# Performance work log

Hardware: AMD Instinct MI355X
Metric: run time of the kernel (lower is better)

The kernel has to match this reference:

```python
import jax, jax.numpy as jnp
import numpy as np

DIM = 2048
N_HEADS = 16
HEAD_DIM = DIM // N_HEADS        # 128
HALF_HD = HEAD_DIM // 2          # 64 (per-context per-head dim)
Q_DIM = DIM // 2                 # 1024
KV_DIM = DIM // 2                # 1024 (n_kv_heads == n_heads)
TOTAL = Q_DIM + 2 * KV_DIM       # 3072
B, S = 2, 2048
EPS = 1e-5


def rmsnorm(x, w, eps=EPS):
    return x * jax.lax.rsqrt(jnp.mean(x * x, axis=-1, keepdims=True) + eps) * w


def rope(x, freqs):
    # x: [B,S,H,D] with D even; freqs: [S, D//2] angles
    xr = x[..., 0::2]
    xi = x[..., 1::2]
    cos = jnp.cos(freqs)[None, :, None, :]
    sin = jnp.sin(freqs)[None, :, None, :]
    out_r = xr * cos - xi * sin
    out_i = xr * sin + xi * cos
    return jnp.stack([out_r, out_i], axis=-1).reshape(x.shape)


def setup_inputs() -> dict:
    key = jax.random.key(0)
    ks = jax.random.split(key, 10)
    inp = {
        "local_c": jax.random.normal(ks[0], (B, S, DIM), jnp.float32),
        "global_c": jax.random.normal(ks[1], (B, S, DIM), jnp.float32),
        "freqs": jax.random.uniform(ks[2], (S, HALF_HD // 2), jnp.float32) * 6.28,
        "W_lc": jax.random.normal(ks[3], (TOTAL, DIM), jnp.float32) * 0.02,
        "W_gc": jax.random.normal(ks[4], (TOTAL, DIM), jnp.float32) * 0.02,
        "q_lc_nw": jnp.ones((Q_DIM,), jnp.float32),
        "k_lc_nw": jnp.ones((KV_DIM,), jnp.float32),
        "q_gc_nw": jnp.ones((Q_DIM,), jnp.float32),
        "k_gc_nw": jnp.ones((KV_DIM,), jnp.float32),
        "q_cat_nw": jnp.ones((HEAD_DIM,), jnp.float32),
        "k_cat_nw": jnp.ones((HEAD_DIM,), jnp.float32),
        "W_lo": jax.random.normal(ks[5], (DIM, 2 * Q_DIM), jnp.float32) * 0.02,
        "b_lo": jnp.zeros((DIM,), jnp.float32),
        "lc_on_w": jnp.ones((DIM,), jnp.float32),
        "W_go": jax.random.normal(ks[6], (DIM, 2 * Q_DIM), jnp.float32) * 0.02,
        "b_go": jnp.zeros((DIM,), jnp.float32),
        "gc_on_w": jnp.ones((DIM,), jnp.float32),
    }
    return inp


def _context_build(x, W, q_nw, k_nw):
    comb = jnp.einsum('bsd,td->bst', x, W)
    q, k, v = jnp.split(comb, [Q_DIM, Q_DIM + KV_DIM], axis=-1)
    q = rmsnorm(q, q_nw).reshape(B, S, N_HEADS, HALF_HD)
    k = rmsnorm(k, k_nw).reshape(B, S, N_HEADS, HALF_HD)
    v = v.reshape(B, S, N_HEADS, HALF_HD)
    return q, k, v


def reference(local_c, global_c, freqs, W_lc, W_gc, q_lc_nw, k_lc_nw, q_gc_nw,
              k_gc_nw, q_cat_nw, k_cat_nw, W_lo, b_lo, lc_on_w, W_go, b_go, gc_on_w):
    q_lc, k_lc, v_lc = _context_build(local_c, W_lc, q_lc_nw, k_lc_nw)
    q_gc, k_gc, v_gc = _context_build(global_c, W_gc, q_gc_nw, k_gc_nw)

    q_lc = rope(q_lc, freqs)
    k_lc = rope(k_lc, freqs)
    q_gc = rope(q_gc, freqs)
    k_gc = rope(k_gc, freqs)

    # concat local+global per head -> [B,S,H,HEAD_DIM], QK-norm over head dim
    xq = rmsnorm(jnp.concatenate([q_lc, q_gc], axis=-1), q_cat_nw)
    xk = rmsnorm(jnp.concatenate([k_lc, k_gc], axis=-1), k_cat_nw)
    xv = jnp.concatenate([v_lc, v_gc], axis=-1)

    scale = 1.0 / np.sqrt(HEAD_DIM)
    scores = jnp.einsum('bqhd,bkhd->bhqk', xq, xk) * scale
    attn = jax.nn.softmax(scores, axis=-1)
    out = jnp.einsum('bhqk,bkhd->bqhd', attn, xv).reshape(B, S, DIM)

    x_lc = rmsnorm(jnp.einsum('bsd,od->bso', out, W_lo) + b_lo, lc_on_w)
    x_gc = rmsnorm(jnp.einsum('bsd,od->bso', out, W_go) + b_go, gc_on_w)
    return (x_lc, x_gc)
```

## Files before the change

### kernel.cpp

```cpp
#include <hip/hip_runtime.h>
#include <hip/hip_bf16.h>

#define DIM 2048
#define NH 16
#define HD 128
#define QD 1024
#define TOT 3072
#define BB 2
#define SS 2048
#define NTOK (BB*SS)
#define EPS 1e-5f

typedef __attribute__((ext_vector_type(4))) float f32x4;
typedef __attribute__((ext_vector_type(8))) short short8;
typedef __attribute__((ext_vector_type(8))) unsigned short u16x8;
typedef __attribute__((ext_vector_type(4))) unsigned short u16x4;

__device__ __forceinline__ float b2f(unsigned short u){
    unsigned int x = ((unsigned int)u) << 16;
    return __builtin_bit_cast(float, x);
}
__device__ __forceinline__ unsigned short f2b(float f){
    unsigned int x = __builtin_bit_cast(unsigned int, f);
    x = (x + 0x7fffu + ((x >> 16) & 1u)) >> 16;
    return (unsigned short)x;
}
__device__ __forceinline__ float exp2_fast(float x){
    float r;
    asm("v_exp_f32 %0, %1" : "=v"(r) : "v"(x));
    return r;
}
__device__ __forceinline__ void store_c(float* p, float v){ *p = v; }
__device__ __forceinline__ void store_c(unsigned short* p, float v){ *p = f2b(v); }

#define MFMA16(a,b,c) __builtin_amdgcn_mfma_f32_16x16x32_bf16((a),(b),(c),0,0,0)

#define GLOAD16(g, l) __builtin_amdgcn_global_load_lds( \
    (const __attribute__((address_space(1))) unsigned int*)(g), \
    (__attribute__((address_space(3))) unsigned int*)(l), 16, 0, 0)

__device__ __forceinline__ void cvt8(const float* __restrict__ s,
                                     unsigned short* __restrict__ d, int i){
    const float4* p = reinterpret_cast<const float4*>(s + (size_t)i * 8);
    float4 a = p[0], b = p[1];
    u16x8 o;
    o[0]=f2b(a.x); o[1]=f2b(a.y); o[2]=f2b(a.z); o[3]=f2b(a.w);
    o[4]=f2b(b.x); o[5]=f2b(b.y); o[6]=f2b(b.z); o[7]=f2b(b.w);
    *reinterpret_cast<u16x8*>(d + (size_t)i * 8) = o;
}

__global__ __launch_bounds__(256) void cvt_multi(
    const float* __restrict__ s0, const float* __restrict__ s1,
    const float* __restrict__ s2, const float* __restrict__ s3,
    const float* __restrict__ s4, const float* __restrict__ s5,
    unsigned short* __restrict__ d0, unsigned short* __restrict__ d1,
    unsigned short* __restrict__ d2, unsigned short* __restrict__ d3,
    unsigned short* __restrict__ d4, unsigned short* __restrict__ d5)
{
    const int N0 = NTOK*DIM/8;
    const int N1 = N0 + NTOK*DIM/8;
    const int N2 = N1 + TOT*DIM/8;
    const int N3 = N2 + TOT*DIM/8;
    const int N4 = N3 + DIM*DIM/8;
    const int N5 = N4 + DIM*DIM/8;
    for (int i = blockIdx.x * blockDim.x + threadIdx.x; i < N5;
         i += gridDim.x * blockDim.x){
        if      (i < N0) cvt8(s0, d0, i);
        else if (i < N1) cvt8(s1, d1, i - N0);
        else if (i < N2) cvt8(s2, d2, i - N1);
        else if (i < N3) cvt8(s3, d3, i - N2);
        else if (i < N4) cvt8(s4, d4, i - N3);
        else             cvt8(s5, d5, i - N4);
    }
}

template<typename OutT>
__global__ __launch_bounds__(256) void gemm_nt(const unsigned short* __restrict__ A0,
                                               const unsigned short* __restrict__ B0,
                                               OutT* __restrict__ C0,
                                               const unsigned short* __restrict__ A1,
                                               const unsigned short* __restrict__ B1,
                                               OutT* __restrict__ C1,
                                               int M, int N, int K){
    __shared__ __attribute__((aligned(16))) unsigned short As[2][128*64];
    __shared__ __attribute__((aligned(16))) unsigned short Bs[2][128*64];
    const int t = threadIdx.x;
    const int lane = t & 63;
    const int w = t >> 6;
    const int wr = w >> 1, wc = w & 1;
    const int gx = gridDim.x;
    const int nwg = gx * gridDim.y;
    int zsel, swz;
    if (gridDim.z == 2){
        const int glin = (int)(blockIdx.z * nwg + blockIdx.y * gx + blockIdx.x);
        const int xcd = glin & 7;
        const int i = glin >> 3;
        zsel = xcd >> 2;
        swz = (xcd & 3) * (nwg >> 2) + i;
    } else {
        const int lin = (int)(blockIdx.y * gx + blockIdx.x);
        const int cpx = nwg >> 3;
        swz = (lin & 7) * cpx + (lin >> 3);
        zsel = 0;
    }
    const unsigned short* A = zsel ? A1 : A0;
    const unsigned short* B = zsel ? B1 : B0;
    OutT* C = zsel ? C1 : C0;
    const int m0 = (swz / gx) * 128, n0 = (swz % gx) * 128;
    const int l16 = lane & 15, lq = lane >> 4;

    f32x4 acc[4][4];
    const f32x4 z = {0.f, 0.f, 0.f, 0.f};
    #pragma unroll
    for (int m = 0; m < 4; ++m)
        #pragma unroll
        for (int n = 0; n < 4; ++n) acc[m][n] = z;

    auto stage = [&](int kt, int bi){
        #pragma unroll
        for (int i = 0; i < 4; ++i){
            int c = t + 256 * i;
            int row = c >> 3, c8 = c & 7;
            int cg = (c8 ^ (row & 7)) * 8;
            GLOAD16(&A[(size_t)(m0 + row) * K + kt + cg],
                    (char*)&As[bi][0] + (size_t)(i * 256 + w * 64) * 16);
            GLOAD16(&B[(size_t)(n0 + row) * K + kt + cg],
                    (char*)&Bs[bi][0] + (size_t)(i * 256 + w * 64) * 16);
        }
    };

    stage(0, 0);
    __syncthreads();
    int cur = 0;

    for (int kt = 0; kt < K; kt += 64){
        if (kt + 64 < K) stage(kt + 64, cur ^ 1);
        #pragma unroll
        for (int kk = 0; kk < 2; ++kk){
            short8 af[4], bf[4];
            #pragma unroll
            for (int m = 0; m < 4; ++m){
                int row = wr*64 + m*16 + l16;
                af[m] = *reinterpret_cast<const short8*>(
                    &As[cur][row*64 + (((kk*4 + lq) ^ (row & 7)) * 8)]);
            }
            #pragma unroll
            for (int n = 0; n < 4; ++n){
                int row = wc*64 + n*16 + l16;
                bf[n] = *reinterpret_cast<const short8*>(
                    &Bs[cur][row*64 + (((kk*4 + lq) ^ (row & 7)) * 8)]);
            }
            #pragma unroll
            for (int m = 0; m < 4; ++m)
                #pragma unroll
                for (int n = 0; n < 4; ++n)
                    acc[m][n] = MFMA16(af[m], bf[n], acc[m][n]);
        }
        __syncthreads();
        cur ^= 1;
    }
    #pragma unroll
    for (int m = 0; m < 4; ++m){
        int grow = m0 + wr*64 + m*16 + lq*4;
        #pragma unroll
        for (int n = 0; n < 4; ++n){
            int gcol = n0 + wc*64 + n*16 + l16;
            #pragma unroll
            for (int r = 0; r < 4; ++r)
                store_c(&C[(size_t)(grow + r) * N + gcol], acc[m][n][r]);
        }
    }
}

__global__ __launch_bounds__(256) void qkv_post(
    const unsigned short* __restrict__ comb_lc, const unsigned short* __restrict__ comb_gc,
    const float* __restrict__ freqs,
    const float* __restrict__ q_lc_nw, const float* __restrict__ k_lc_nw,
    const float* __restrict__ q_gc_nw, const float* __restrict__ k_gc_nw,
    const float* __restrict__ q_cat_nw, const float* __restrict__ k_cat_nw,
    unsigned short* __restrict__ xq, unsigned short* __restrict__ xk,
    unsigned short* __restrict__ xv)
{
    __shared__ float qcat[16][128];
    __shared__ float kcat[16][128];
    __shared__ float rbuf[4][4];
    const int tok = blockIdx.x;
    const int s = tok & (SS - 1);
    const unsigned short* clc = comb_lc + (size_t)tok * TOT;
    const unsigned short* cgc = comb_gc + (size_t)tok * TOT;
    const int t = threadIdx.x;
    const int lane = t & 63, w = t >> 6;

    const unsigned short* segs[4] = { clc, clc + QD, cgc, cgc + QD };
    const float* wts[4] = { q_lc_nw, k_lc_nw, q_gc_nw, k_gc_nw };

    float ss4[4];
    #pragma unroll
    for (int sg = 0; sg < 4; ++sg){
        u16x4 v = *reinterpret_cast<const u16x4*>(segs[sg] + t * 4);
        float acc = 0.f;
        #pragma unroll
        for (int j = 0; j < 4; ++j){ float f = b2f(v[j]); acc += f * f; }
        ss4[sg] = acc;
    }
    #pragma unroll
    for (int sg = 0; sg < 4; ++sg){
        float v = ss4[sg];
        #pragma unroll
        for (int o = 32; o >= 1; o >>= 1) v += __shfl_xor(v, o);
        if (lane == 0) rbuf[sg][w] = v;
    }
    __syncthreads();
    float rms[4];
    #pragma unroll
    for (int sg = 0; sg < 4; ++sg){
        float tot = rbuf[sg][0] + rbuf[sg][1] + rbuf[sg][2] + rbuf[sg][3];
        rms[sg] = rsqrtf(tot * (1.f / QD) + EPS);
    }

    #pragma unroll
    for (int sg = 0; sg < 4; ++sg){
        const unsigned short* seg = segs[sg];
        const float* wt = wts[sg];
        const float rf = rms[sg];
        float (*dst)[128] = (sg == 0 || sg == 2) ? qcat : kcat;
        const int coff = (sg >= 2) ? 64 : 0;
        #pragma unroll
        for (int pi = 0; pi < 2; ++pi){
            int p = t + pi * 256;
            int h = p >> 5, j = p & 31;
            int idx = h * 64 + 2 * j;
            float xr = b2f(seg[idx])     * rf * wt[idx];
            float xi = b2f(seg[idx + 1]) * rf * wt[idx + 1];
            float fr = freqs[(size_t)s * 32 + j];
            float cs = __cosf(fr), sn = __sinf(fr);
            dst[h][coff + 2*j]     = xr * cs - xi * sn;
            dst[h][coff + 2*j + 1] = xr * sn + xi * cs;
        }
    }

    {
        int i0 = t * 4;
        int h = i0 >> 6, d = i0 & 63;
        u16x4 vlc = *reinterpret_cast<const u16x4*>(clc + 2048 + i0);
        u16x4 vgc = *reinterpret_cast<const u16x4*>(cgc + 2048 + i0);
        *reinterpret_cast<u16x4*>(&xv[(size_t)tok * DIM + h * 128 + d])      = vlc;
        *reinterpret_cast<u16x4*>(&xv[(size_t)tok * DIM + h * 128 + 64 + d]) = vgc;
    }
    __syncthreads();

    {
        int h = t >> 4, sub = t & 15;
        float sq = 0.f, sk = 0.f;
        #pragma unroll
        for (int j = 0; j < 8; ++j){
            float a = qcat[h][sub*8 + j]; sq += a * a;
            float b = kcat[h][sub*8 + j]; sk += b * b;
        }
        #pragma unroll
        for (int o = 1; o < 16; o <<= 1){ sq += __shfl_xor(sq, o); sk += __shfl_xor(sk, o); }
        float rq = rsqrtf(sq * (1.f / 128) + EPS);
        float rk = rsqrtf(sk * (1.f / 128) + EPS);
        u16x8 oq, ok;
        #pragma unroll
        for (int j = 0; j < 8; ++j){
            int d = sub*8 + j;
            oq[j] = f2b(qcat[h][d] * rq * q_cat_nw[d]);
            ok[j] = f2b(kcat[h][d] * rk * k_cat_nw[d]);
        }
        *reinterpret_cast<u16x8*>(&xq[(size_t)tok * DIM + h * 128 + sub*8]) = oq;
        *reinterpret_cast<u16x8*>(&xk[(size_t)tok * DIM + h * 128 + sub*8]) = ok;
    }
}

__global__ __launch_bounds__(256) void transpose_v(const unsigned short* __restrict__ xv,
                                                   unsigned short* __restrict__ xvT){
    __shared__ unsigned short tile[128][129];
    const int blk = blockIdx.x;
    const int st = blk & 15;
    const int bh = blk >> 4;
    const int b = bh >> 4, h = bh & 15;
    const int t = threadIdx.x;
    const int s0 = st * 128;
    #pragma unroll
    for (int i = 0; i < 8; ++i){
        int c = t + 256 * i;
        int r = c >> 4, dc = c & 15;
        u16x8 v = *reinterpret_cast<const u16x8*>(&xv[((size_t)(b*SS + s0 + r)) * DIM + h*HD + dc*8]);
        #pragma unroll
        for (int j = 0; j < 8; ++j) tile[r][dc*8 + j] = v[j];
    }
    __syncthreads();
    #pragma unroll
    for (int i = 0; i < 8; ++i){
        int c = t + 256 * i;
        int d = c >> 4, sc = c & 15;
        u16x8 o;
        #pragma unroll
        for (int j = 0; j < 8; ++j) o[j] = tile[sc*8 + j][d];
        *reinterpret_cast<u16x8*>(&xvT[((size_t)bh * HD + d) * SS + s0 + sc*8]) = o;
    }
}

__global__ __launch_bounds__(256) void attn_fwd(const unsigned short* __restrict__ xq,
                                                const unsigned short* __restrict__ xk,
                                                const unsigned short* __restrict__ xvT,
                                                unsigned short* __restrict__ attn_out){
    __shared__ __attribute__((aligned(16))) unsigned short Kl[2][64 * 128];
    __shared__ __attribute__((aligned(16))) unsigned short Vt[2][128 * 64];
    __shared__ __attribute__((aligned(16))) unsigned short Pl[4][16 * 64];
    const int blk = ((int)blockIdx.x & 7) * 128 + ((int)blockIdx.x >> 3);
    const int qt = blk & 31, h = (blk >> 5) & 15, b = blk >> 9;
    const int t = threadIdx.x, lane = t & 63, w = t >> 6;
    const int l16 = lane & 15, lq = lane >> 4;
    const float scale2 = 0.12751744751f;
    const float MBIAS = 16.6f;
    const int qbase = qt * 64 + w * 16;

    short8 qf[4];
    #pragma unroll
    for (int ks = 0; ks < 4; ++ks)
        qf[ks] = *reinterpret_cast<const short8*>(
            &xq[((size_t)(b*SS + qbase + l16)) * DIM + h*HD + ks*32 + lq*8]);

    float psum = 0.f;
    f32x4 O[8];
    const f32x4 z = {0.f, 0.f, 0.f, 0.f};
    #pragma unroll
    for (int dn = 0; dn < 8; ++dn) O[dn] = z;

    const size_t kbase = (size_t)(b*SS) * DIM + h*HD;
    const size_t vbase = ((size_t)(b*NH + h)) * HD * SS;

    auto stage = [&](int kt, int bi){
        #pragma unroll
        for (int i = 0; i < 4; ++i){
            int slot = i*256 + w*64 + lane;
            int r = slot >> 4, dc = slot & 15;
            GLOAD16(&xk[kbase + (size_t)(kt*64 + r) * DIM + ((dc ^ (r & 7)) * 8)],
                    (char*)&Kl[bi][0] + (size_t)(i*256 + w*64) * 16);
            int d = slot >> 3, kc = slot & 7;
            GLOAD16(&xvT[vbase + (size_t)d * SS + kt*64 + ((kc ^ (d & 7)) * 8)],
                    (char*)&Vt[bi][0] + (size_t)(i*256 + w*64) * 16);
        }
    };

    stage(0, 0);
    __syncthreads();

    unsigned short* P = Pl[w];
    int cur = 0;

    for (int kt = 0; kt < SS/64; ++kt){
        if (kt + 1 < SS/64) stage(kt + 1, cur ^ 1);

        const unsigned short* Kc = Kl[cur];
        const unsigned short* Vc = Vt[cur];

        f32x4 St[4];
        #pragma unroll
        for (int kn = 0; kn < 4; ++kn) St[kn] = z;
        __builtin_amdgcn_s_setprio(1);
        #pragma unroll
        for (int kn = 0; kn < 4; ++kn){
            int kr = kn*16 + l16;
            #pragma unroll
            for (int ks = 0; ks < 4; ++ks){
                short8 ak = *reinterpret_cast<const short8*>(
                    &Kc[kr*128 + (((ks*4 + lq) ^ (kr & 7)) * 8)]);
                St[kn] = MFMA16(ak, qf[ks], St[kn]);
            }
        }
        __builtin_amdgcn_s_setprio(0);

        uint2 pk[4];
        #pragma unroll
        for (int kn = 0; kn < 4; ++kn){
            float p0 = exp2_fast(St[kn][0]*scale2 - MBIAS);
            float p1 = exp2_fast(St[kn][1]*scale2 - MBIAS);
            float p2 = exp2_fast(St[kn][2]*scale2 - MBIAS);
            float p3 = exp2_fast(St[kn][3]*scale2 - MBIAS);
            psum += (p0 + p1) + (p2 + p3);
            unsigned lo, hi;
            asm("v_cvt_pk_bf16_f32 %0, %1, %2" : "=v"(lo) : "v"(p0), "v"(p1));
            asm("v_cvt_pk_bf16_f32 %0, %1, %2" : "=v"(hi) : "v"(p2), "v"(p3));
            pk[kn].x = lo; pk[kn].y = hi;
        }

        #pragma unroll
        for (int kn = 0; kn < 4; ++kn){
            int kk = kn >> 1;
            int lqp = (kn & 1)*2 + (lq >> 1);
            *reinterpret_cast<uint2*>(&P[(kk*64 + lqp*16 + l16)*8 + (lq & 1)*4]) = pk[kn];
        }
        asm volatile("s_waitcnt lgkmcnt(0)" ::: "memory");
        __builtin_amdgcn_sched_barrier(0);

        __builtin_amdgcn_s_setprio(1);
        #pragma unroll
        for (int kk = 0; kk < 2; ++kk){
            short8 pb = *reinterpret_cast<const short8*>(&P[(kk*64 + lq*16 + l16)*8]);
            #pragma unroll
            for (int dn = 0; dn < 8; ++dn){
                int dr = dn*16 + l16;
                short8 av = *reinterpret_cast<const short8*>(
                    &Vc[dr*64 + (((kk*4 + lq) ^ (dr & 7)) * 8)]);
                O[dn] = MFMA16(av, pb, O[dn]);
            }
        }
        __builtin_amdgcn_s_setprio(0);

        __syncthreads();
        cur ^= 1;
    }

    psum += __shfl_xor(psum, 16);
    psum += __shfl_xor(psum, 32);
    float inv = 1.f / psum;
    #pragma unroll
    for (int dn = 0; dn < 8; ++dn){
        u16x4 o4;
        #pragma unroll
        for (int r = 0; r < 4; ++r) o4[r] = f2b(O[dn][r] * inv);
        *reinterpret_cast<u16x4*>(
            &attn_out[((size_t)(b*SS + qbase + l16)) * DIM + h*HD + dn*16 + lq*4]) = o4;
    }
}

__global__ __launch_bounds__(256) void proj_norm2(const unsigned short* __restrict__ proj,
                                                  const float* __restrict__ b_lo,
                                                  const float* __restrict__ b_go,
                                                  const float* __restrict__ w_lc,
                                                  const float* __restrict__ w_gc,
                                                  float* __restrict__ out){
    __shared__ float buf[DIM];
    __shared__ float rbuf[4];
    const int half = blockIdx.x >> 12;
    const int row  = blockIdx.x & (NTOK - 1);
    const unsigned short* p = proj + (size_t)row * (2*DIM) + (size_t)half * DIM;
    const float* bias = half ? b_go : b_lo;
    const float* w    = half ? w_gc : w_lc;
    float* o = out + (size_t)half * NTOK * DIM + (size_t)row * DIM;
    const int t = threadIdx.x;
    const int lane = t & 63, wv = t >> 6;
    float ssq = 0.f;
    #pragma unroll
    for (int i = 0; i < 8; ++i){
        int c = t + i * 256;
        float v = b2f(p[c]) + bias[c];
        buf[c] = v;
        ssq += v * v;
    }
    #pragma unroll
    for (int o2 = 32; o2 >= 1; o2 >>= 1) ssq += __shfl_xor(ssq, o2);
    if (lane == 0) rbuf[wv] = ssq;
    __syncthreads();
    float tot = rbuf[0] + rbuf[1] + rbuf[2] + rbuf[3];
    float rr = rsqrtf(tot * (1.f / DIM) + EPS);
    #pragma unroll
    for (int i = 0; i < 8; ++i){
        int c = t + i * 256;
        o[c] = buf[c] * rr * w[c];
    }
}

extern "C" void kernel_launch(void* const* d_in, const int* in_sizes, int n_in,
                              void* d_out, int out_size, void* d_ws, size_t ws_size,
                              hipStream_t stream)
{
    const float* local_c  = (const float*)d_in[0];
    const float* global_c = (const float*)d_in[1];
    const float* freqs    = (const float*)d_in[2];
    const float* W_lc     = (const float*)d_in[3];
    const float* W_gc     = (const float*)d_in[4];
    const float* q_lc_nw  = (const float*)d_in[5];
    const float* k_lc_nw  = (const float*)d_in[6];
    const float* q_gc_nw  = (const float*)d_in[7];
    const float* k_gc_nw  = (const float*)d_in[8];
    const float* q_cat_nw = (const float*)d_in[9];
    const float* k_cat_nw = (const float*)d_in[10];
    const float* W_lo     = (const float*)d_in[11];
    const float* b_lo     = (const float*)d_in[12];
    const float* lc_on_w  = (const float*)d_in[13];
    const float* W_go     = (const float*)d_in[14];
    const float* b_go     = (const float*)d_in[15];
    const float* gc_on_w  = (const float*)d_in[16];
    float* out = (float*)d_out;

    char* ws = (char*)d_ws;
    const size_t SZ_WLO  = (size_t)DIM * DIM * 2;
    const size_t SZ_WLC  = (size_t)TOT * DIM * 2;
    const size_t SZ_TOK2 = (size_t)NTOK * DIM * 2;
    const size_t SZ_COMB = (size_t)NTOK * TOT * 2;

    unsigned short* Wlo_b  = (unsigned short*)(ws);
    unsigned short* Wgo_b  = (unsigned short*)(ws + SZ_WLO);
    char*           slotW  = ws + 2*SZ_WLO;
    unsigned short* Wlc_b  = (unsigned short*)(slotW);
    unsigned short* Wgc_b  = (unsigned short*)(slotW + SZ_WLC);
    unsigned short* xv     = (unsigned short*)(slotW);
    char*           slotE  = ws + 2*SZ_WLO + 2*SZ_WLC;
    char*           slotF  = slotE + SZ_TOK2;
    unsigned short* xb_lc  = (unsigned short*)slotE;
    unsigned short* xb_gc  = (unsigned short*)slotF;
    unsigned short* xq     = (unsigned short*)slotE;
    unsigned short* xk     = (unsigned short*)slotF;
    unsigned short* proj   = (unsigned short*)slotE;
    char*           slotG  = slotF + SZ_TOK2;
    char*           slotH  = slotG + SZ_COMB;
    unsigned short* comb_lc= (unsigned short*)slotG;
    unsigned short* comb_gc= (unsigned short*)slotH;
    unsigned short* xvT    = (unsigned short*)slotG;
    unsigned short* attn_o = (unsigned short*)slotH;
    (void)ws_size;

    cvt_multi<<<2048, 256, 0, stream>>>(local_c, global_c, W_lc, W_gc, W_lo, W_go,
                                        xb_lc, xb_gc, Wlc_b, Wgc_b, Wlo_b, Wgo_b);

    dim3 g1(TOT / 128, NTOK / 128, 2);
    gemm_nt<unsigned short><<<g1, 256, 0, stream>>>(xb_lc, Wlc_b, comb_lc,
                                                    xb_gc, Wgc_b, comb_gc, NTOK, TOT, DIM);

    qkv_post<<<NTOK, 256, 0, stream>>>(comb_lc, comb_gc, freqs,
                                       q_lc_nw, k_lc_nw, q_gc_nw, k_gc_nw,
                                       q_cat_nw, k_cat_nw, xq, xk, xv);

    transpose_v<<<512, 256, 0, stream>>>(xv, xvT);

    attn_fwd<<<1024, 256, 0, stream>>>(xq, xk, xvT, attn_o);

    dim3 g2(2 * DIM / 128, NTOK / 128, 1);
    gemm_nt<unsigned short><<<g2, 256, 0, stream>>>(attn_o, Wlo_b, proj,
                                                    attn_o, Wlo_b, proj, NTOK, 2*DIM, DIM);

    proj_norm2<<<2*NTOK, 256, 0, stream>>>(proj, b_lo, b_go, lc_on_w, gc_on_w, out);
}
```

Measured before the change: 388.1 us.

## Double query rows per attention block and triple-buffer B tiles in GEMM

The attention kernel now has each wave process 32 query rows (two groups of 16) instead of 16. This halves the grid to 512 blocks, so each K/V tile staged in shared memory and each V fragment read serves twice as many MFMAs. The GEMM loads its B operand two tiles ahead into a third LDS buffer and replaces __syncthreads with explicit vmcnt waits plus s_barrier, aiming to hide more global-load latency. In exchange, the attention kernel holds more accumulator registers and has fewer blocks to fill the GPU. The GEMM's extra LDS buffer may lower occupancy.

```diff
diff --git a/kernel.cpp b/kernel.cpp
--- a/kernel.cpp
+++ b/kernel.cpp
@@ -83,7 +83,7 @@
                                                OutT* __restrict__ C1,
                                                int M, int N, int K){
     __shared__ __attribute__((aligned(16))) unsigned short As[2][128*64];
-    __shared__ __attribute__((aligned(16))) unsigned short Bs[2][128*64];
+    __shared__ __attribute__((aligned(16))) unsigned short Bs[3][128*64];
     const int t = threadIdx.x;
     const int lane = t & 63;
     const int w = t >> 6;
@@ -116,25 +116,39 @@
         #pragma unroll
         for (int n = 0; n < 4; ++n) acc[m][n] = z;
 
-    auto stage = [&](int kt, int bi){
+    auto stageA = [&](int kt, int bi){
         #pragma unroll
         for (int i = 0; i < 4; ++i){
             int c = t + 256 * i;
             int row = c >> 3, c8 = c & 7;
             int cg = (c8 ^ (row & 7)) * 8;
-            GLOAD16(&A[(size_t)(m0 + row) * K + kt + cg],
+            GLOAD16(&A[(size_t)(m0 + row) * K + kt*64 + cg],
                     (char*)&As[bi][0] + (size_t)(i * 256 + w * 64) * 16);
-            GLOAD16(&B[(size_t)(n0 + row) * K + kt + cg],
+        }
+    };
+    auto stageB = [&](int kt, int bi){
+        #pragma unroll
+        for (int i = 0; i < 4; ++i){
+            int c = t + 256 * i;
+            int row = c >> 3, c8 = c & 7;
+            int cg = (c8 ^ (row & 7)) * 8;
+            GLOAD16(&B[(size_t)(n0 + row) * K + kt*64 + cg],
                     (char*)&Bs[bi][0] + (size_t)(i * 256 + w * 64) * 16);
         }
     };
 
-    stage(0, 0);
-    __syncthreads();
-    int cur = 0;
-
-    for (int kt = 0; kt < K; kt += 64){
-        if (kt + 64 < K) stage(kt + 64, cur ^ 1);
+    const int NTt = K >> 6;
+    stageA(0, 0); stageB(0, 0);
+    if (NTt > 1) stageB(1, 1);
+    if (NTt > 1) asm volatile("s_waitcnt vmcnt(4)" ::: "memory");
+    else         asm volatile("s_waitcnt vmcnt(0)" ::: "memory");
+    __builtin_amdgcn_s_barrier();
+    __builtin_amdgcn_sched_barrier(0);
+
+    int a0 = 0, b0 = 0, b1 = 1, b2 = 2;
+    for (int kt = 0; kt < NTt; ++kt){
+        if (kt + 1 < NTt) stageA(kt + 1, a0 ^ 1);
+        if (kt + 2 < NTt) stageB(kt + 2, b2);
         #pragma unroll
         for (int kk = 0; kk < 2; ++kk){
             short8 af[4], bf[4];
@@ -142,13 +156,13 @@
             for (int m = 0; m < 4; ++m){
                 int row = wr*64 + m*16 + l16;
                 af[m] = *reinterpret_cast<const short8*>(
-                    &As[cur][row*64 + (((kk*4 + lq) ^ (row & 7)) * 8)]);
+                    &As[a0][row*64 + (((kk*4 + lq) ^ (row & 7)) * 8)]);
             }
             #pragma unroll
             for (int n = 0; n < 4; ++n){
                 int row = wc*64 + n*16 + l16;
                 bf[n] = *reinterpret_cast<const short8*>(
-                    &Bs[cur][row*64 + (((kk*4 + lq) ^ (row & 7)) * 8)]);
+                    &Bs[b0][row*64 + (((kk*4 + lq) ^ (row & 7)) * 8)]);
             }
             #pragma unroll
             for (int m = 0; m < 4; ++m)
@@ -156,8 +170,14 @@
                 for (int n = 0; n < 4; ++n)
                     acc[m][n] = MFMA16(af[m], bf[n], acc[m][n]);
         }
-        __syncthreads();
-        cur ^= 1;
+        if (kt + 1 < NTt){
+            if (kt + 2 < NTt) asm volatile("s_waitcnt vmcnt(4)" ::: "memory");
+            else              asm volatile("s_waitcnt vmcnt(0)" ::: "memory");
+            __builtin_amdgcn_s_barrier();
+            __builtin_amdgcn_sched_barrier(0);
+        }
+        a0 ^= 1;
+        int tmp = b0; b0 = b1; b1 = b2; b2 = tmp;
     }
     #pragma unroll
     for (int m = 0; m < 4; ++m){
@@ -308,26 +328,30 @@
                                                 unsigned short* __restrict__ attn_out){
     __shared__ __attribute__((aligned(16))) unsigned short Kl[2][64 * 128];
     __shared__ __attribute__((aligned(16))) unsigned short Vt[2][128 * 64];
-    __shared__ __attribute__((aligned(16))) unsigned short Pl[4][16 * 64];
-    const int blk = ((int)blockIdx.x & 7) * 128 + ((int)blockIdx.x >> 3);
-    const int qt = blk & 31, h = (blk >> 5) & 15, b = blk >> 9;
+    __shared__ __attribute__((aligned(16))) unsigned short Pl[4][2][16 * 64];
+    const int blk = ((int)blockIdx.x & 7) * 64 + ((int)blockIdx.x >> 3);
+    const int qt = blk & 15, h = (blk >> 4) & 15, b = blk >> 8;
     const int t = threadIdx.x, lane = t & 63, w = t >> 6;
     const int l16 = lane & 15, lq = lane >> 4;
     const float scale2 = 0.12751744751f;
     const float MBIAS = 16.6f;
-    const int qbase = qt * 64 + w * 16;
-
-    short8 qf[4];
-    #pragma unroll
-    for (int ks = 0; ks < 4; ++ks)
-        qf[ks] = *reinterpret_cast<const short8*>(
-            &xq[((size_t)(b*SS + qbase + l16)) * DIM + h*HD + ks*32 + lq*8]);
-
-    float psum = 0.f;
-    f32x4 O[8];
+    const int qbase = qt * 128 + w * 32;
+
+    short8 qf[2][4];
+    #pragma unroll
+    for (int g = 0; g < 2; ++g)
+        #pragma unroll
+        for (int ks = 0; ks < 4; ++ks)
+            qf[g][ks] = *reinterpret_cast<const short8*>(
+                &xq[((size_t)(b*SS + qbase + g*16 + l16)) * DIM + h*HD + ks*32 + lq*8]);
+
+    float psum[2] = {0.f, 0.f};
+    f32x4 O[2][8];
     const f32x4 z = {0.f, 0.f, 0.f, 0.f};
     #pragma unroll
-    for (int dn = 0; dn < 8; ++dn) O[dn] = z;
+    for (int g = 0; g < 2; ++g)
+        #pragma unroll
+        for (int dn = 0; dn < 8; ++dn) O[g][dn] = z;
 
     const size_t kbase = (size_t)(b*SS) * DIM + h*HD;
     const size_t vbase = ((size_t)(b*NH + h)) * HD * SS;
@@ -348,7 +372,6 @@
     stage(0, 0);
     __syncthreads();
 
-    unsigned short* P = Pl[w];
     int cur = 0;
 
     for (int kt = 0; kt < SS/64; ++kt){
@@ -357,41 +380,40 @@
         const unsigned short* Kc = Kl[cur];
         const unsigned short* Vc = Vt[cur];
 
-        f32x4 St[4];
-        #pragma unroll
-        for (int kn = 0; kn < 4; ++kn) St[kn] = z;
-        __builtin_amdgcn_s_setprio(1);
-        #pragma unroll
-        for (int kn = 0; kn < 4; ++kn){
-            int kr = kn*16 + l16;
-            #pragma unroll
-            for (int ks = 0; ks < 4; ++ks){
-                short8 ak = *reinterpret_cast<const short8*>(
-                    &Kc[kr*128 + (((ks*4 + lq) ^ (kr & 7)) * 8)]);
-                St[kn] = MFMA16(ak, qf[ks], St[kn]);
+        #pragma unroll
+        for (int g = 0; g < 2; ++g){
+            f32x4 St[4];
+            #pragma unroll
+            for (int kn = 0; kn < 4; ++kn) St[kn] = z;
+            __builtin_amdgcn_s_setprio(1);
+            #pragma unroll
+            for (int kn = 0; kn < 4; ++kn){
+                int kr = kn*16 + l16;
+                #pragma unroll
+                for (int ks = 0; ks < 4; ++ks){
+                    short8 ak = *reinterpret_cast<const short8*>(
+                        &Kc[kr*128 + (((ks*4 + lq) ^ (kr & 7)) * 8)]);
+                    St[kn] = MFMA16(ak, qf[g][ks], St[kn]);
+                }
             }
-        }
-        __builtin_amdgcn_s_setprio(0);
-
-        uint2 pk[4];
-        #pragma unroll
-        for (int kn = 0; kn < 4; ++kn){
-            float p0 = exp2_fast(St[kn][0]*scale2 - MBIAS);
-            float p1 = exp2_fast(St[kn][1]*scale2 - MBIAS);
-            float p2 = exp2_fast(St[kn][2]*scale2 - MBIAS);
-            float p3 = exp2_fast(St[kn][3]*scale2 - MBIAS);
-            psum += (p0 + p1) + (p2 + p3);
-            unsigned lo, hi;
-            asm("v_cvt_pk_bf16_f32 %0, %1, %2" : "=v"(lo) : "v"(p0), "v"(p1));
-            asm("v_cvt_pk_bf16_f32 %0, %1, %2" : "=v"(hi) : "v"(p2), "v"(p3));
-            pk[kn].x = lo; pk[kn].y = hi;
-        }
-
-        #pragma unroll
-        for (int kn = 0; kn < 4; ++kn){
-            int kk = kn >> 1;
-            int lqp = (kn & 1)*2 + (lq >> 1);
-            *reinterpret_cast<uint2*>(&P[(kk*64 + lqp*16 + l16)*8 + (lq & 1)*4]) = pk[kn];
+            __builtin_amdgcn_s_setprio(0);
+
+            unsigned short* P = Pl[w][g];
+            #pragma unroll
+            for (int kn = 0; kn < 4; ++kn){
+                float p0 = exp2_fast(St[kn][0]*scale2 - MBIAS);
+                float p1 = exp2_fast(St[kn][1]*scale2 - MBIAS);
+                float p2 = exp2_fast(St[kn][2]*scale2 - MBIAS);
+                float p3 = exp2_fast(St[kn][3]*scale2 - MBIAS);
+                psum[g] += (p0 + p1) + (p2 + p3);
+                unsigned lo, hi;
+                asm("v_cvt_pk_bf16_f32 %0, %1, %2" : "=v"(lo) : "v"(p0), "v"(p1));
+                asm("v_cvt_pk_bf16_f32 %0, %1, %2" : "=v"(hi) : "v"(p2), "v"(p3));
+                uint2 pk2; pk2.x = lo; pk2.y = hi;
+                int kk = kn >> 1;
+                int lqp = (kn & 1)*2 + (lq >> 1);
+                *reinterpret_cast<uint2*>(&P[(kk*64 + lqp*16 + l16)*8 + (lq & 1)*4]) = pk2;
+            }
         }
         asm volatile("s_waitcnt lgkmcnt(0)" ::: "memory");
         __builtin_amdgcn_sched_barrier(0);
@@ -399,13 +421,15 @@
         __builtin_amdgcn_s_setprio(1);
         #pragma unroll
         for (int kk = 0; kk < 2; ++kk){
-            short8 pb = *reinterpret_cast<const short8*>(&P[(kk*64 + lq*16 + l16)*8]);
+            short8 pb0 = *reinterpret_cast<const short8*>(&Pl[w][0][(kk*64 + lq*16 + l16)*8]);
+            short8 pb1 = *reinterpret_cast<const short8*>(&Pl[w][1][(kk*64 + lq*16 + l16)*8]);
             #pragma unroll
             for (int dn = 0; dn < 8; ++dn){
                 int dr = dn*16 + l16;
                 short8 av = *reinterpret_cast<const short8*>(
                     &Vc[dr*64 + (((kk*4 + lq) ^ (dr & 7)) * 8)]);
-                O[dn] = MFMA16(av, pb, O[dn]);
+                O[0][dn] = MFMA16(av, pb0, O[0][dn]);
+                O[1][dn] = MFMA16(av, pb1, O[1][dn]);
             }
         }
         __builtin_amdgcn_s_setprio(0);
@@ -414,16 +438,20 @@
         cur ^= 1;
     }
 
-    psum += __shfl_xor(psum, 16);
-    psum += __shfl_xor(psum, 32);
-    float inv = 1.f / psum;
-    #pragma unroll
-    for (int dn = 0; dn < 8; ++dn){
-        u16x4 o4;
-        #pragma unroll
-        for (int r = 0; r < 4; ++r) o4[r] = f2b(O[dn][r] * inv);
-        *reinterpret_cast<u16x4*>(
-            &attn_out[((size_t)(b*SS + qbase + l16)) * DIM + h*HD + dn*16 + lq*4]) = o4;
+    #pragma unroll
+    for (int g = 0; g < 2; ++g){
+        float ps = psum[g];
+        ps += __shfl_xor(ps, 16);
+        ps += __shfl_xor(ps, 32);
+        float inv = 1.f / ps;
+        #pragma unroll
+        for (int dn = 0; dn < 8; ++dn){
+            u16x4 o4;
+            #pragma unroll
+            for (int r = 0; r < 4; ++r) o4[r] = f2b(O[g][dn][r] * inv);
+            *reinterpret_cast<u16x4*>(
+                &attn_out[((size_t)(b*SS + qbase + g*16 + l16)) * DIM + h*HD + dn*16 + lq*4]) = o4;
+        }
     }
 }
 
@@ -527,7 +555,7 @@
 
     transpose_v<<<512, 256, 0, stream>>>(xv, xvT);
 
-    attn_fwd<<<1024, 256, 0, stream>>>(xq, xk, xvT, attn_o);
+    attn_fwd<<<512, 256, 0, stream>>>(xq, xk, xvT, attn_o);
 
     dim3 g2(2 * DIM / 128, NTOK / 128, 1);
     gemm_nt<unsigned short><<<g2, 256, 0, stream>>>(attn_o, Wlo_b, proj,
```

Result: faster. 373.4 us (-3.8%).
